# Optimization experiments

Measured on AMD Instinct MI355X. Metric: run time of the kernel, lower is better.

The kernel has to match this reference:

```python
import jax, jax.numpy as jnp
import numpy as np

N_NODES = 50000
N_EDGES = 800000
D_IN, D_HID, D_OUT = 128, 128, 64


def _gcn_conv(x, row, col, W, b, num_nodes):
    # Linear (no bias in lin; bias added after aggregation)
    h = x @ W  # [N, d_out]
    # degree over destination (col), includes self-loops
    deg = jax.ops.segment_sum(jnp.ones_like(col, dtype=h.dtype), col, num_segments=num_nodes)
    dis = jnp.where(deg > 0, deg ** -0.5, 0.0)  # deg^{-1/2}, inf -> 0
    norm = dis[row] * dis[col]  # [E+N]
    msg = h[row] * norm[:, None]  # gather + scale
    out = jax.ops.segment_sum(msg, col, num_segments=num_nodes)  # scatter-add
    return out + b


def setup_inputs() -> dict:
    key = jax.random.key(0)
    k1, k2, k3, k4 = jax.random.split(key, 4)
    x = jax.random.normal(k1, (N_NODES, D_IN), dtype=jnp.float32)
    edge_index = jax.random.randint(k2, (2, N_EDGES), 0, N_NODES, dtype=jnp.int32)
    # glorot-like init for linear weights
    W1 = jax.random.normal(k3, (D_IN, D_HID), dtype=jnp.float32) * (2.0 / (D_IN + D_HID)) ** 0.5
    W2 = jax.random.normal(k4, (D_HID, D_OUT), dtype=jnp.float32) * (2.0 / (D_HID + D_OUT)) ** 0.5
    b1 = jnp.zeros((D_HID,), dtype=jnp.float32)
    b2 = jnp.zeros((D_OUT,), dtype=jnp.float32)
    return {"x": x, "edge_index": edge_index, "W1": W1, "b1": b1, "W2": W2, "b2": b2}


def reference(x, edge_index, W1, b1, W2, b2):
    n = x.shape[0]
    # add self-loops
    loops = jnp.arange(n, dtype=edge_index.dtype)
    row = jnp.concatenate([edge_index[0], loops])
    col = jnp.concatenate([edge_index[1], loops])
    h = _gcn_conv(x, row, col, W1, b1, n)
    h = jax.nn.relu(h)  # dropout is identity in eval mode
    out = _gcn_conv(h, row, col, W2, b2, n)
    return out
```

## Files before the change

### kernel.cpp

```cpp
#include <hip/hip_runtime.h>

#define BSH 7
#define BMSK 127
#define NB 391
#define ROWSH 13
#define RCH 7
#define SEG (NB * RCH)
#define NBLK 256
#define BINCAP 3072

typedef __attribute__((ext_vector_type(8))) short short8;
typedef __attribute__((ext_vector_type(4))) float f32x4;
typedef __attribute__((ext_vector_type(4))) unsigned int u32x4;

static inline size_t alignup(size_t x) { return (x + 255) & ~(size_t)255; }

__device__ __forceinline__ unsigned short f2bf(float f) {
    unsigned int u = __float_as_uint(f);
    u = (u + 0x7fffu + ((u >> 16) & 1u)) >> 16;
    return (unsigned short)u;
}

__global__ __launch_bounds__(256) void k_prep(const float* __restrict__ W1,
                                              const float* __restrict__ W2,
                                              unsigned short* __restrict__ Wt1,
                                              unsigned short* __restrict__ Wt2) {
    int i = blockIdx.x * 256 + threadIdx.x;
    if (i < 128 * 128) { int k = i >> 7, c = i & 127; Wt1[(size_t)c * 128 + k] = f2bf(W1[i]); }
    if (i < 128 * 64)  { int k = i >> 6, c = i & 63;  Wt2[(size_t)c * 128 + k] = f2bf(W2[i]); }
}

__global__ __launch_bounds__(256) void k_front(const float* __restrict__ x,
                                               const unsigned short* __restrict__ Wt1,
                                               unsigned short* __restrict__ hs1, int M,
                                               const int* __restrict__ colp,
                                               const int* __restrict__ rowp, int nE,
                                               unsigned* __restrict__ counts, int G1) {
    if ((int)blockIdx.x >= G1) {
        int blk = blockIdx.x - G1;
        __shared__ unsigned h[SEG];
        for (int i = threadIdx.x; i < SEG; i += 256) h[i] = 0;
        __syncthreads();
        int chunk = (nE + NBLK - 1) / NBLK;
        int e0 = blk * chunk, e1 = min(nE, e0 + chunk);
        for (int e = e0 + (int)threadIdx.x; e < e1; e += 256) {
            int c = colp[e], r = rowp[e];
            atomicAdd(&h[(c >> BSH) * RCH + (r >> ROWSH)], 1u);
        }
        __syncthreads();
        for (int i = threadIdx.x; i < SEG; i += 256) counts[(size_t)i * NBLK + blk] = h[i];
        return;
    }
    const int NT = 8;
    const int lane = threadIdx.x & 63;
    const int wave = threadIdx.x >> 6;
    const int m0 = blockIdx.x * 64 + wave * 16;
    const int lrow = lane & 15;
    const int lk = lane >> 4;
    int arow = m0 + lrow;
    if (arow >= M) arow = M - 1;

    f32x4 acc[NT];
#pragma unroll
    for (int t = 0; t < NT; ++t) acc[t] = (f32x4){0.f, 0.f, 0.f, 0.f};

#pragma unroll
    for (int k0 = 0; k0 < 4; ++k0) {
        const int kb = k0 * 32 + lk * 8;
        const float* ap = &x[(size_t)arow * 128 + kb];
        f32x4 v0 = __builtin_nontemporal_load((const f32x4*)ap);
        f32x4 v1 = __builtin_nontemporal_load((const f32x4*)(ap + 4));
        short8 afrag;
#pragma unroll
        for (int q = 0; q < 4; ++q) {
            afrag[q] = (short)f2bf(v0[q]);
            afrag[4 + q] = (short)f2bf(v1[q]);
        }
#pragma unroll
        for (int t = 0; t < NT; ++t) {
            const int bcol = t * 16 + lrow;
            short8 bfrag = *(const short8*)&Wt1[(size_t)bcol * 128 + kb];
            acc[t] = __builtin_amdgcn_mfma_f32_16x16x32_bf16(afrag, bfrag, acc[t], 0, 0, 0);
        }
    }
#pragma unroll
    for (int i = 0; i < 4; ++i) {
        int row = m0 + lk * 4 + i;
        if (row < M) {
#pragma unroll
            for (int t = 0; t < NT; ++t)
                hs1[(size_t)row * 128 + t * 16 + lrow] = f2bf(acc[t][i]);
        }
    }
}

__global__ __launch_bounds__(NBLK) void k_scanA(unsigned* __restrict__ counts,
                                                unsigned* __restrict__ segtot) {
    int seg = blockIdx.x, t = threadIdx.x;
    __shared__ unsigned ps[NBLK];
    unsigned s = counts[(size_t)seg * NBLK + t];
    ps[t] = s;
    __syncthreads();
    for (int d = 1; d < NBLK; d <<= 1) {
        unsigned v = (t >= d) ? ps[t - d] : 0u;
        __syncthreads();
        ps[t] += v;
        __syncthreads();
    }
    counts[(size_t)seg * NBLK + t] = ps[t] - s;
    if (t == NBLK - 1) segtot[seg] = ps[NBLK - 1];
}

__global__ __launch_bounds__(256) void k_scanB(const unsigned* __restrict__ segtot,
                                               unsigned* __restrict__ segbase,
                                               unsigned* __restrict__ edgebase, int nE) {
    __shared__ unsigned ls[SEG];
    __shared__ unsigned ts[256];
    int t = threadIdx.x;
    for (int i = t; i < SEG; i += 256) ls[i] = segtot[i];
    __syncthreads();
    const int CH = (SEG + 255) / 256;
    unsigned s = 0;
#pragma unroll
    for (int j = 0; j < CH; ++j) {
        int idx = t * CH + j;
        if (idx < SEG) s += ls[idx];
    }
    ts[t] = s;
    __syncthreads();
    for (int d = 1; d < 256; d <<= 1) {
        unsigned v = (t >= d) ? ts[t - d] : 0u;
        __syncthreads();
        ts[t] += v;
        __syncthreads();
    }
    unsigned run = ts[t] - s;
    unsigned loc[CH > 0 ? CH : 1];
#pragma unroll
    for (int j = 0; j < CH; ++j) {
        int idx = t * CH + j;
        if (idx < SEG) { unsigned v = ls[idx]; loc[j] = run; segbase[idx] = run; run += v; }
    }
    __syncthreads();
#pragma unroll
    for (int j = 0; j < CH; ++j) {
        int idx = t * CH + j;
        if (idx < SEG) ls[idx] = loc[j];
    }
    __syncthreads();
    for (int b = t; b < NB; b += 256) edgebase[b] = ls[b * RCH];
    if (t == 0) edgebase[NB] = (unsigned)nE;
}

__global__ __launch_bounds__(256) void k_scatter(const int* __restrict__ colp,
                                                 const int* __restrict__ rowp, int nE,
                                                 const unsigned* __restrict__ counts,
                                                 const unsigned* __restrict__ segbase,
                                                 unsigned* __restrict__ pairs) {
    __shared__ unsigned cur[SEG];
    int blk = blockIdx.x;
    for (int i = threadIdx.x; i < SEG; i += 256)
        cur[i] = segbase[i] + counts[(size_t)i * NBLK + blk];
    __syncthreads();
    int chunk = (nE + NBLK - 1) / NBLK;
    int e0 = blk * chunk, e1 = min(nE, e0 + chunk);
    for (int e = e0 + (int)threadIdx.x; e < e1; e += 256) {
        int c = colp[e], r = rowp[e];
        unsigned pos = atomicAdd(&cur[(c >> BSH) * RCH + (r >> ROWSH)], 1u);
        pairs[pos] = ((unsigned)r << BSH) | (unsigned)(c & BMSK);
    }
}

__global__ __launch_bounds__(256) void k_binbuild(const unsigned* __restrict__ pairs,
                                                  const unsigned* __restrict__ edgebase,
                                                  unsigned* __restrict__ csr,
                                                  unsigned* __restrict__ off,
                                                  float* __restrict__ dis, int n) {
    __shared__ unsigned lp[BINCAP];
    __shared__ unsigned lr[BINCAP];
    __shared__ unsigned hist[128];
    __shared__ unsigned scn[128];
    int b = blockIdx.x, t = threadIdx.x;
    unsigned e0 = edgebase[b], e1 = edgebase[b + 1];
    unsigned ec = e1 - e0;
    if (ec > BINCAP) ec = BINCAP;
    if (t < 128) hist[t] = 0;
    __syncthreads();
    for (unsigned i = t; i < ec; i += 256) {
        unsigned v = pairs[e0 + i];
        lp[i] = v;
        atomicAdd(&hist[v & BMSK], 1u);
    }
    __syncthreads();
    unsigned hv = (t < 128) ? hist[t] : 0u;
    if (t < 128) scn[t] = hv;
    __syncthreads();
    for (int d = 1; d < 128; d <<= 1) {
        unsigned v = (t < 128 && t >= d) ? scn[t - d] : 0u;
        __syncthreads();
        if (t < 128) scn[t] += v;
        __syncthreads();
    }
    unsigned ex = (t < 128) ? scn[t] - hv : 0u;
    int node = (b << BSH) + t;
    if (t < 128 && node < n) {
        off[node] = e0 + ex;
        dis[node] = rsqrtf((float)(hv + 1));
    }
    if (b == NB - 1 && t == 0) off[n] = e1;
    __syncthreads();
    if (t < 128) scn[t] = ex;
    __syncthreads();
    for (unsigned i = t; i < ec; i += 256) {
        unsigned v = lp[i];
        unsigned pos = atomicAdd(&scn[v & BMSK], 1u);
        lr[pos] = v >> BSH;
    }
    __syncthreads();
    for (unsigned i = t; i < ec; i += 256) csr[e0 + i] = lr[i];
}

__device__ __forceinline__ void acc8s(float a[8], u32x4 u, float d) {
    a[0] = fmaf(__uint_as_float(u[0] << 16), d, a[0]);
    a[1] = fmaf(__uint_as_float(u[0] & 0xffff0000u), d, a[1]);
    a[2] = fmaf(__uint_as_float(u[1] << 16), d, a[2]);
    a[3] = fmaf(__uint_as_float(u[1] & 0xffff0000u), d, a[3]);
    a[4] = fmaf(__uint_as_float(u[2] << 16), d, a[4]);
    a[5] = fmaf(__uint_as_float(u[2] & 0xffff0000u), d, a[5]);
    a[6] = fmaf(__uint_as_float(u[3] << 16), d, a[6]);
    a[7] = fmaf(__uint_as_float(u[3] & 0xffff0000u), d, a[7]);
}

__device__ __forceinline__ void acc8(float a[8], u32x4 u) {
    a[0] += __uint_as_float(u[0] << 16);
    a[1] += __uint_as_float(u[0] & 0xffff0000u);
    a[2] += __uint_as_float(u[1] << 16);
    a[3] += __uint_as_float(u[1] & 0xffff0000u);
    a[4] += __uint_as_float(u[2] << 16);
    a[5] += __uint_as_float(u[2] & 0xffff0000u);
    a[6] += __uint_as_float(u[3] << 16);
    a[7] += __uint_as_float(u[3] & 0xffff0000u);
}

__global__ __launch_bounds__(256) void k_fuse2(const unsigned short* __restrict__ hs1,
                                               const unsigned* __restrict__ csr,
                                               const unsigned* __restrict__ off,
                                               const float* __restrict__ dis,
                                               const float* __restrict__ b1,
                                               const unsigned short* __restrict__ Wt2,
                                               unsigned short* __restrict__ hs2, int n) {
    __shared__ unsigned short st[16 * 136];
    const int tid = threadIdx.x;
    int vloc = tid >> 4;
    int c = tid & 15;
    int v = blockIdx.x * 16 + vloc;
    if (v >= n) v = n - 1;

    const u32x4* h4 = (const u32x4*)hs1;
    size_t base = (size_t)v * 16 + c;
    unsigned s = off[v], e = off[v + 1];
    float dv = dis[v];

    float a[8];
#pragma unroll
    for (int j = 0; j < 8; ++j) a[j] = 0.f;
    acc8s(a, h4[base], dv);

    unsigned i = s;
    for (; i + 4 <= e; i += 4) {
        unsigned r0 = csr[i], r1 = csr[i + 1], r2 = csr[i + 2], r3 = csr[i + 3];
        float d0 = dis[r0], d1 = dis[r1], d2 = dis[r2], d3 = dis[r3];
        u32x4 m0 = h4[(size_t)r0 * 16 + c];
        u32x4 m1 = h4[(size_t)r1 * 16 + c];
        u32x4 m2 = h4[(size_t)r2 * 16 + c];
        u32x4 m3 = h4[(size_t)r3 * 16 + c];
        acc8s(a, m0, d0); acc8s(a, m1, d1); acc8s(a, m2, d2); acc8s(a, m3, d3);
    }
    for (; i < e; ++i) {
        unsigned r = csr[i];
        acc8s(a, h4[(size_t)r * 16 + c], dis[r]);
    }

    u32x4 pk;
#pragma unroll
    for (int q = 0; q < 4; ++q) {
        float lo = fmaxf(a[2 * q] * dv + b1[c * 8 + 2 * q], 0.f);
        float hi = fmaxf(a[2 * q + 1] * dv + b1[c * 8 + 2 * q + 1], 0.f);
        pk[q] = (unsigned)f2bf(lo) | ((unsigned)f2bf(hi) << 16);
    }
    *(u32x4*)&st[vloc * 136 + c * 8] = pk;
    __syncthreads();

    const int lane = tid & 63;
    const int wave = tid >> 6;
    const int lrow = lane & 15;
    const int lk = lane >> 4;
    f32x4 acc = (f32x4){0.f, 0.f, 0.f, 0.f};
#pragma unroll
    for (int k0 = 0; k0 < 4; ++k0) {
        const int kb = k0 * 32 + lk * 8;
        short8 afrag = *(const short8*)&st[lrow * 136 + kb];
        const int bcol = wave * 16 + lrow;
        short8 bfrag = *(const short8*)&Wt2[(size_t)bcol * 128 + kb];
        acc = __builtin_amdgcn_mfma_f32_16x16x32_bf16(afrag, bfrag, acc, 0, 0, 0);
    }
#pragma unroll
    for (int i2 = 0; i2 < 4; ++i2) {
        int row = blockIdx.x * 16 + lk * 4 + i2;
        if (row < n) {
            float sc = dis[row];
            hs2[(size_t)row * 64 + wave * 16 + lrow] = f2bf(acc[i2] * sc);
        }
    }
}

__global__ __launch_bounds__(256) void k_gather2(const unsigned short* __restrict__ hs,
                                                 const unsigned* __restrict__ csr,
                                                 const unsigned* __restrict__ off,
                                                 const float* __restrict__ dis,
                                                 const float* __restrict__ bias,
                                                 float* __restrict__ outp, int n) {
    int v = blockIdx.x * 32 + (int)(threadIdx.x >> 3);
    int c = threadIdx.x & 7;
    if (v >= n) return;
    const u32x4* h4 = (const u32x4*)hs;
    size_t base = (size_t)v * 8 + c;

    unsigned s = off[v], e = off[v + 1];
    float dv = dis[v];

    float a[8];
#pragma unroll
    for (int j = 0; j < 8; ++j) a[j] = 0.f;
    acc8(a, h4[base]);

    unsigned i = s;
    for (; i + 4 <= e; i += 4) {
        unsigned r0 = csr[i], r1 = csr[i + 1], r2 = csr[i + 2], r3 = csr[i + 3];
        u32x4 m0 = h4[(size_t)r0 * 8 + c];
        u32x4 m1 = h4[(size_t)r1 * 8 + c];
        u32x4 m2 = h4[(size_t)r2 * 8 + c];
        u32x4 m3 = h4[(size_t)r3 * 8 + c];
        acc8(a, m0); acc8(a, m1); acc8(a, m2); acc8(a, m3);
    }
    for (; i < e; ++i) acc8(a, h4[(size_t)csr[i] * 8 + c]);

    float rr[8];
#pragma unroll
    for (int j = 0; j < 8; ++j) rr[j] = a[j] * dv + bias[c * 8 + j];
    f32x4 lov = {rr[0], rr[1], rr[2], rr[3]};
    f32x4 hiv = {rr[4], rr[5], rr[6], rr[7]};
    __builtin_nontemporal_store(lov, (f32x4*)&outp[(size_t)v * 64 + c * 8]);
    __builtin_nontemporal_store(hiv, (f32x4*)&outp[(size_t)v * 64 + c * 8 + 4]);
}

extern "C" void kernel_launch(void* const* d_in, const int* in_sizes, int n_in,
                              void* d_out, int out_size, void* d_ws, size_t ws_size,
                              hipStream_t stream) {
    const float* x  = (const float*)d_in[0];
    const int*   ei = (const int*)d_in[1];
    const float* W1 = (const float*)d_in[2];
    const float* b1 = (const float*)d_in[3];
    const float* W2 = (const float*)d_in[4];
    const float* b2 = (const float*)d_in[5];

    const int Din = 128;
    const int Nn = in_sizes[0] / Din;
    const int E  = in_sizes[1] / 2;
    const int* rowp = ei;
    const int* colp = ei + E;

    char* ws = (char*)d_ws;
    size_t off_ = 0;
    unsigned*       counts   = (unsigned*)(ws + off_);       off_ = alignup(off_ + (size_t)SEG * NBLK * 4);
    unsigned*       segtot   = (unsigned*)(ws + off_);       off_ = alignup(off_ + (size_t)SEG * 4);
    unsigned*       segbase  = (unsigned*)(ws + off_);       off_ = alignup(off_ + (size_t)SEG * 4);
    unsigned*       edgebase = (unsigned*)(ws + off_);       off_ = alignup(off_ + (size_t)(NB + 1) * 4);
    unsigned*       pairs    = (unsigned*)(ws + off_);       off_ = alignup(off_ + (size_t)E * 4);
    unsigned*       csr      = (unsigned*)(ws + off_);       off_ = alignup(off_ + (size_t)E * 4);
    unsigned*       offv     = (unsigned*)(ws + off_);       off_ = alignup(off_ + (size_t)(Nn + 1) * 4);
    float*          dis      = (float*)(ws + off_);          off_ = alignup(off_ + (size_t)Nn * 4);
    unsigned short* Wt1      = (unsigned short*)(ws + off_); off_ = alignup(off_ + 128 * 128 * 2);
    unsigned short* Wt2      = (unsigned short*)(ws + off_); off_ = alignup(off_ + 128 * 64 * 2);
    unsigned short* hs1      = (unsigned short*)(ws + off_); off_ = alignup(off_ + (size_t)Nn * 128 * 2);
    unsigned short* hs2      = (unsigned short*)(ws + off_); off_ = alignup(off_ + (size_t)Nn * 64 * 2);
    float*          outp     = (float*)d_out;

    const int G1 = (Nn + 63) / 64;

    k_prep<<<64, 256, 0, stream>>>(W1, W2, Wt1, Wt2);

    k_front<<<G1 + NBLK, 256, 0, stream>>>(x, Wt1, hs1, Nn, colp, rowp, E, counts, G1);

    k_scanA<<<SEG, NBLK, 0, stream>>>(counts, segtot);
    k_scanB<<<1, 256, 0, stream>>>(segtot, segbase, edgebase, E);

    k_scatter<<<NBLK, 256, 0, stream>>>(colp, rowp, E, counts, segbase, pairs);
    k_binbuild<<<NB, 256, 0, stream>>>(pairs, edgebase, csr, offv, dis, Nn);

    k_fuse2<<<(Nn + 15) / 16, 256, 0, stream>>>(hs1, csr, offv, dis, b1, Wt2, hs2, Nn);

    k_gather2<<<(Nn + 31) / 32, 256, 0, stream>>>(hs2, csr, offv, dis, b2, outp, Nn);
}
```

Baseline: 117.6 us.

## Merge prep into histogram, fold global scan into scatter, fuse scatter with GEMM

Weight conversion now runs as extra blocks of the histogram kernel. The single-block global scan is removed: every scatter block recomputes the segment prefix sum redundantly, and the same launch also carries the first-layer GEMM blocks. This cuts two kernel launches and their serialization points. It also lets the x@W1 GEMM overlap the edge scatter. Separately, the gather loops in both aggregation kernels are unrolled to 8 edges per iteration for more memory-level parallelism, at the cost of more registers and redundant scan work per block.

```diff
diff --git a/kernel.cpp b/kernel.cpp
--- a/kernel.cpp
+++ b/kernel.cpp
@@ -21,40 +21,114 @@
     return (unsigned short)u;
 }
 
-__global__ __launch_bounds__(256) void k_prep(const float* __restrict__ W1,
+__global__ __launch_bounds__(256) void k_hist(const int* __restrict__ colp,
+                                              const int* __restrict__ rowp, int nE,
+                                              unsigned* __restrict__ counts,
+                                              const float* __restrict__ W1,
                                               const float* __restrict__ W2,
                                               unsigned short* __restrict__ Wt1,
                                               unsigned short* __restrict__ Wt2) {
-    int i = blockIdx.x * 256 + threadIdx.x;
-    if (i < 128 * 128) { int k = i >> 7, c = i & 127; Wt1[(size_t)c * 128 + k] = f2bf(W1[i]); }
-    if (i < 128 * 64)  { int k = i >> 6, c = i & 63;  Wt2[(size_t)c * 128 + k] = f2bf(W2[i]); }
-}
-
-__global__ __launch_bounds__(256) void k_front(const float* __restrict__ x,
-                                               const unsigned short* __restrict__ Wt1,
-                                               unsigned short* __restrict__ hs1, int M,
-                                               const int* __restrict__ colp,
-                                               const int* __restrict__ rowp, int nE,
-                                               unsigned* __restrict__ counts, int G1) {
-    if ((int)blockIdx.x >= G1) {
-        int blk = blockIdx.x - G1;
-        __shared__ unsigned h[SEG];
-        for (int i = threadIdx.x; i < SEG; i += 256) h[i] = 0;
+    int blk = blockIdx.x;
+    if (blk >= NBLK) {
+        int i = (blk - NBLK) * 256 + threadIdx.x;
+        if (i < 128 * 128) { int k = i >> 7, c = i & 127; Wt1[(size_t)c * 128 + k] = f2bf(W1[i]); }
+        if (i < 128 * 64)  { int k = i >> 6, c = i & 63;  Wt2[(size_t)c * 128 + k] = f2bf(W2[i]); }
+        return;
+    }
+    __shared__ unsigned h[SEG];
+    for (int i = threadIdx.x; i < SEG; i += 256) h[i] = 0;
+    __syncthreads();
+    int chunk = (nE + NBLK - 1) / NBLK;
+    int e0 = blk * chunk, e1 = min(nE, e0 + chunk);
+    for (int e = e0 + (int)threadIdx.x; e < e1; e += 256) {
+        int c = colp[e], r = rowp[e];
+        atomicAdd(&h[(c >> BSH) * RCH + (r >> ROWSH)], 1u);
+    }
+    __syncthreads();
+    for (int i = threadIdx.x; i < SEG; i += 256) counts[(size_t)i * NBLK + blk] = h[i];
+}
+
+__global__ __launch_bounds__(NBLK) void k_scanA(unsigned* __restrict__ counts,
+                                                unsigned* __restrict__ segtot) {
+    int seg = blockIdx.x, t = threadIdx.x;
+    __shared__ unsigned ps[NBLK];
+    unsigned s = counts[(size_t)seg * NBLK + t];
+    ps[t] = s;
+    __syncthreads();
+    for (int d = 1; d < NBLK; d <<= 1) {
+        unsigned v = (t >= d) ? ps[t - d] : 0u;
+        __syncthreads();
+        ps[t] += v;
+        __syncthreads();
+    }
+    counts[(size_t)seg * NBLK + t] = ps[t] - s;
+    if (t == NBLK - 1) segtot[seg] = ps[NBLK - 1];
+}
+
+__global__ __launch_bounds__(256) void k_scatgemm(const int* __restrict__ colp,
+                                                  const int* __restrict__ rowp, int nE,
+                                                  const unsigned* __restrict__ counts,
+                                                  const unsigned* __restrict__ segtot,
+                                                  unsigned* __restrict__ pairs,
+                                                  unsigned* __restrict__ edgebase,
+                                                  const float* __restrict__ x,
+                                                  const unsigned short* __restrict__ Wt1,
+                                                  unsigned short* __restrict__ hs1, int M) {
+    if ((int)blockIdx.x < NBLK) {
+        __shared__ unsigned sb[SEG];
+        __shared__ unsigned ts[256];
+        int t = threadIdx.x, blk = blockIdx.x;
+        for (int i = t; i < SEG; i += 256) sb[i] = segtot[i];
+        __syncthreads();
+        const int CH = (SEG + 255) / 256;
+        unsigned s = 0;
+#pragma unroll
+        for (int j = 0; j < CH; ++j) {
+            int idx = t * CH + j;
+            if (idx < SEG) s += sb[idx];
+        }
+        ts[t] = s;
+        __syncthreads();
+        for (int d = 1; d < 256; d <<= 1) {
+            unsigned v = (t >= d) ? ts[t - d] : 0u;
+            __syncthreads();
+            ts[t] += v;
+            __syncthreads();
+        }
+        unsigned run = ts[t] - s;
+        unsigned loc[CH > 0 ? CH : 1];
+#pragma unroll
+        for (int j = 0; j < CH; ++j) {
+            int idx = t * CH + j;
+            if (idx < SEG) { unsigned v = sb[idx]; loc[j] = run; run += v; }
+        }
+        __syncthreads();
+#pragma unroll
+        for (int j = 0; j < CH; ++j) {
+            int idx = t * CH + j;
+            if (idx < SEG) sb[idx] = loc[j];
+        }
+        __syncthreads();
+        if (blk == 0) {
+            for (int b = t; b < NB; b += 256) edgebase[b] = sb[b * RCH];
+            if (t == 0) edgebase[NB] = (unsigned)nE;
+        }
+        for (int i = t; i < SEG; i += 256) sb[i] += counts[(size_t)i * NBLK + blk];
         __syncthreads();
         int chunk = (nE + NBLK - 1) / NBLK;
         int e0 = blk * chunk, e1 = min(nE, e0 + chunk);
-        for (int e = e0 + (int)threadIdx.x; e < e1; e += 256) {
+        for (int e = e0 + (int)t; e < e1; e += 256) {
             int c = colp[e], r = rowp[e];
-            atomicAdd(&h[(c >> BSH) * RCH + (r >> ROWSH)], 1u);
-        }
-        __syncthreads();
-        for (int i = threadIdx.x; i < SEG; i += 256) counts[(size_t)i * NBLK + blk] = h[i];
+            unsigned pos = atomicAdd(&sb[(c >> BSH) * RCH + (r >> ROWSH)], 1u);
+            pairs[pos] = ((unsigned)r << BSH) | (unsigned)(c & BMSK);
+        }
         return;
     }
     const int NT = 8;
+    const int bid = blockIdx.x - NBLK;
     const int lane = threadIdx.x & 63;
     const int wave = threadIdx.x >> 6;
-    const int m0 = blockIdx.x * 64 + wave * 16;
+    const int m0 = bid * 64 + wave * 16;
     const int lrow = lane & 15;
     const int lk = lane >> 4;
     int arow = m0 + lrow;
@@ -91,83 +165,6 @@
             for (int t = 0; t < NT; ++t)
                 hs1[(size_t)row * 128 + t * 16 + lrow] = f2bf(acc[t][i]);
         }
-    }
-}
-
-__global__ __launch_bounds__(NBLK) void k_scanA(unsigned* __restrict__ counts,
-                                                unsigned* __restrict__ segtot) {
-    int seg = blockIdx.x, t = threadIdx.x;
-    __shared__ unsigned ps[NBLK];
-    unsigned s = counts[(size_t)seg * NBLK + t];
-    ps[t] = s;
-    __syncthreads();
-    for (int d = 1; d < NBLK; d <<= 1) {
-        unsigned v = (t >= d) ? ps[t - d] : 0u;
-        __syncthreads();
-        ps[t] += v;
-        __syncthreads();
-    }
-    counts[(size_t)seg * NBLK + t] = ps[t] - s;
-    if (t == NBLK - 1) segtot[seg] = ps[NBLK - 1];
-}
-
-__global__ __launch_bounds__(256) void k_scanB(const unsigned* __restrict__ segtot,
-                                               unsigned* __restrict__ segbase,
-                                               unsigned* __restrict__ edgebase, int nE) {
-    __shared__ unsigned ls[SEG];
-    __shared__ unsigned ts[256];
-    int t = threadIdx.x;
-    for (int i = t; i < SEG; i += 256) ls[i] = segtot[i];
-    __syncthreads();
-    const int CH = (SEG + 255) / 256;
-    unsigned s = 0;
-#pragma unroll
-    for (int j = 0; j < CH; ++j) {
-        int idx = t * CH + j;
-        if (idx < SEG) s += ls[idx];
-    }
-    ts[t] = s;
-    __syncthreads();
-    for (int d = 1; d < 256; d <<= 1) {
-        unsigned v = (t >= d) ? ts[t - d] : 0u;
-        __syncthreads();
-        ts[t] += v;
-        __syncthreads();
-    }
-    unsigned run = ts[t] - s;
-    unsigned loc[CH > 0 ? CH : 1];
-#pragma unroll
-    for (int j = 0; j < CH; ++j) {
-        int idx = t * CH + j;
-        if (idx < SEG) { unsigned v = ls[idx]; loc[j] = run; segbase[idx] = run; run += v; }
-    }
-    __syncthreads();
-#pragma unroll
-    for (int j = 0; j < CH; ++j) {
-        int idx = t * CH + j;
-        if (idx < SEG) ls[idx] = loc[j];
-    }
-    __syncthreads();
-    for (int b = t; b < NB; b += 256) edgebase[b] = ls[b * RCH];
-    if (t == 0) edgebase[NB] = (unsigned)nE;
-}
-
-__global__ __launch_bounds__(256) void k_scatter(const int* __restrict__ colp,
-                                                 const int* __restrict__ rowp, int nE,
-                                                 const unsigned* __restrict__ counts,
-                                                 const unsigned* __restrict__ segbase,
-                                                 unsigned* __restrict__ pairs) {
-    __shared__ unsigned cur[SEG];
-    int blk = blockIdx.x;
-    for (int i = threadIdx.x; i < SEG; i += 256)
-        cur[i] = segbase[i] + counts[(size_t)i * NBLK + blk];
-    __syncthreads();
-    int chunk = (nE + NBLK - 1) / NBLK;
-    int e0 = blk * chunk, e1 = min(nE, e0 + chunk);
-    for (int e = e0 + (int)threadIdx.x; e < e1; e += 256) {
-        int c = colp[e], r = rowp[e];
-        unsigned pos = atomicAdd(&cur[(c >> BSH) * RCH + (r >> ROWSH)], 1u);
-        pairs[pos] = ((unsigned)r << BSH) | (unsigned)(c & BMSK);
     }
 }
 
@@ -267,7 +264,20 @@
     acc8s(a, h4[base], dv);
 
     unsigned i = s;
-    for (; i + 4 <= e; i += 4) {
+    for (; i + 8 <= e; i += 8) {
+        unsigned r[8];
+        float d[8];
+        u32x4 m[8];
+#pragma unroll
+        for (int j = 0; j < 8; ++j) r[j] = csr[i + j];
+#pragma unroll
+        for (int j = 0; j < 8; ++j) d[j] = dis[r[j]];
+#pragma unroll
+        for (int j = 0; j < 8; ++j) m[j] = h4[(size_t)r[j] * 16 + c];
+#pragma unroll
+        for (int j = 0; j < 8; ++j) acc8s(a, m[j], d[j]);
+    }
+    if (i + 4 <= e) {
         unsigned r0 = csr[i], r1 = csr[i + 1], r2 = csr[i + 2], r3 = csr[i + 3];
         float d0 = dis[r0], d1 = dis[r1], d2 = dis[r2], d3 = dis[r3];
         u32x4 m0 = h4[(size_t)r0 * 16 + c];
@@ -275,6 +285,7 @@
         u32x4 m2 = h4[(size_t)r2 * 16 + c];
         u32x4 m3 = h4[(size_t)r3 * 16 + c];
         acc8s(a, m0, d0); acc8s(a, m1, d1); acc8s(a, m2, d2); acc8s(a, m3, d3);
+        i += 4;
     }
     for (; i < e; ++i) {
         unsigned r = csr[i];
@@ -335,13 +346,24 @@
     acc8(a, h4[base]);
 
     unsigned i = s;
-    for (; i + 4 <= e; i += 4) {
+    for (; i + 8 <= e; i += 8) {
+        unsigned r[8];
+        u32x4 m[8];
+#pragma unroll
+        for (int j = 0; j < 8; ++j) r[j] = csr[i + j];
+#pragma unroll
+        for (int j = 0; j < 8; ++j) m[j] = h4[(size_t)r[j] * 8 + c];
+#pragma unroll
+        for (int j = 0; j < 8; ++j) acc8(a, m[j]);
+    }
+    if (i + 4 <= e) {
         unsigned r0 = csr[i], r1 = csr[i + 1], r2 = csr[i + 2], r3 = csr[i + 3];
         u32x4 m0 = h4[(size_t)r0 * 8 + c];
         u32x4 m1 = h4[(size_t)r1 * 8 + c];
         u32x4 m2 = h4[(size_t)r2 * 8 + c];
         u32x4 m3 = h4[(size_t)r3 * 8 + c];
         acc8(a, m0); acc8(a, m1); acc8(a, m2); acc8(a, m3);
+        i += 4;
     }
     for (; i < e; ++i) acc8(a, h4[(size_t)csr[i] * 8 + c]);
 
@@ -374,7 +396,6 @@
     size_t off_ = 0;
     unsigned*       counts   = (unsigned*)(ws + off_);       off_ = alignup(off_ + (size_t)SEG * NBLK * 4);
     unsigned*       segtot   = (unsigned*)(ws + off_);       off_ = alignup(off_ + (size_t)SEG * 4);
-    unsigned*       segbase  = (unsigned*)(ws + off_);       off_ = alignup(off_ + (size_t)SEG * 4);
     unsigned*       edgebase = (unsigned*)(ws + off_);       off_ = alignup(off_ + (size_t)(NB + 1) * 4);
     unsigned*       pairs    = (unsigned*)(ws + off_);       off_ = alignup(off_ + (size_t)E * 4);
     unsigned*       csr      = (unsigned*)(ws + off_);       off_ = alignup(off_ + (size_t)E * 4);
@@ -388,14 +409,10 @@
 
     const int G1 = (Nn + 63) / 64;
 
-    k_prep<<<64, 256, 0, stream>>>(W1, W2, Wt1, Wt2);
-
-    k_front<<<G1 + NBLK, 256, 0, stream>>>(x, Wt1, hs1, Nn, colp, rowp, E, counts, G1);
-
+    k_hist<<<NBLK + 64, 256, 0, stream>>>(colp, rowp, E, counts, W1, W2, Wt1, Wt2);
     k_scanA<<<SEG, NBLK, 0, stream>>>(counts, segtot);
-    k_scanB<<<1, 256, 0, stream>>>(segtot, segbase, edgebase, E);
-
-    k_scatter<<<NBLK, 256, 0, stream>>>(colp, rowp, E, counts, segbase, pairs);
+    k_scatgemm<<<NBLK + G1, 256, 0, stream>>>(colp, rowp, E, counts, segtot,
+                                              pairs, edgebase, x, Wt1, hs1, Nn);
     k_binbuild<<<NB, 256, 0, stream>>>(pairs, edgebase, csr, offv, dis, Nn);
 
     k_fuse2<<<(Nn + 15) / 16, 256, 0, stream>>>(hs1, csr, offv, dis, b1, Wt2, hs2, Nn);
```

Result: slower. 120.1 us (+2.1%).
